# Optimization experiments

Measured on AMD Instinct MI355X. Metric: run time of the kernel, lower is better.

## Reference

```python
import jax, jax.numpy as jnp
import numpy as np

LATENT = 512
HIDDEN = 1024
SLOTS = 16
BATCH = 256
HORIZON = 64


def _linear(x, W, b):
    # torch nn.Linear convention: W [out, in]
    return x @ W.T + b


def _lstm_cell(x, h, c, w_ih, w_hh, b_ih, b_hh):
    # PyTorch gate order: i, f, g, o
    gates = x @ w_ih.T + b_ih + h @ w_hh.T + b_hh
    i, f, g, o = jnp.split(gates, 4, axis=-1)
    i = jax.nn.sigmoid(i)
    f = jax.nn.sigmoid(f)
    g = jnp.tanh(g)
    o = jax.nn.sigmoid(o)
    c_new = f * c + i * g
    h_new = o * jnp.tanh(c_new)
    return h_new, c_new


def setup_inputs() -> dict:
    key = jax.random.key(0)
    ks = iter(jax.random.split(key, 32))

    def rn(shape, scale=None):
        k = next(ks)
        s = scale if scale is not None else 1.0 / np.sqrt(shape[-1])
        return jax.random.normal(k, shape, dtype=jnp.float32) * s

    inp = {
        "current_state": jax.random.normal(next(ks), (BATCH, LATENT), dtype=jnp.float32),
        "horizon": HORIZON,
        # ContextMemory
        "memory": jax.random.normal(next(ks), (SLOTS, HIDDEN), dtype=jnp.float32) * 0.01,
        "q_W": rn((HIDDEN, LATENT)), "q_b": jnp.zeros((HIDDEN,), jnp.float32),
        "k_W": rn((HIDDEN, HIDDEN)), "k_b": jnp.zeros((HIDDEN,), jnp.float32),
        "v_W": rn((HIDDEN, HIDDEN)), "v_b": jnp.zeros((HIDDEN,), jnp.float32),
        "mo_W": rn((LATENT, HIDDEN)), "mo_b": jnp.zeros((LATENT,), jnp.float32),
        # prior_generator: Linear(2L->H), ReLU, Linear(H->L)
        "pg_W1": rn((HIDDEN, 2 * LATENT)), "pg_b1": jnp.zeros((HIDDEN,), jnp.float32),
        "pg_W2": rn((LATENT, HIDDEN)), "pg_b2": jnp.zeros((LATENT,), jnp.float32),
        # LSTM layer 0 (input LATENT) and layer 1 (input HIDDEN)
        "w_ih0": rn((4 * HIDDEN, LATENT)), "w_hh0": rn((4 * HIDDEN, HIDDEN)),
        "b_ih0": jnp.zeros((4 * HIDDEN,), jnp.float32), "b_hh0": jnp.zeros((4 * HIDDEN,), jnp.float32),
        "w_ih1": rn((4 * HIDDEN, HIDDEN)), "w_hh1": rn((4 * HIDDEN, HIDDEN)),
        "b_ih1": jnp.zeros((4 * HIDDEN,), jnp.float32), "b_hh1": jnp.zeros((4 * HIDDEN,), jnp.float32),
        # output_proj: Linear(H->H), ReLU, Linear(H->L)
        "op_W1": rn((HIDDEN, HIDDEN)), "op_b1": jnp.zeros((HIDDEN,), jnp.float32),
        "op_W2": rn((LATENT, HIDDEN)), "op_b2": jnp.zeros((LATENT,), jnp.float32),
    }
    return inp


def reference(current_state, horizon, memory,
              q_W, q_b, k_W, k_b, v_W, v_b, mo_W, mo_b,
              pg_W1, pg_b1, pg_W2, pg_b2,
              w_ih0, w_hh0, b_ih0, b_hh0,
              w_ih1, w_hh1, b_ih1, b_hh1,
              op_W1, op_b1, op_W2, op_b2):
    B = current_state.shape[0]

    # --- ContextMemory.read ---
    q = _linear(current_state, q_W, q_b)          # [B, M]
    k = _linear(memory, k_W, k_b)                 # [S, M]
    v = _linear(memory, v_W, v_b)                 # [S, M]
    scores = (q @ k.T) / jnp.sqrt(jnp.float32(HIDDEN))  # [B, S]
    weights = jax.nn.softmax(scores, axis=-1)
    ctx = weights @ v                             # [B, M]
    context = _linear(ctx, mo_W, mo_b)            # [B, L]

    # --- prior_generator ---
    combined = jnp.concatenate([current_state, context], axis=-1)
    prior = _linear(jax.nn.relu(_linear(combined, pg_W1, pg_b1)), pg_W2, pg_b2)

    h0 = jnp.zeros((B, HIDDEN), jnp.float32)
    c0 = jnp.zeros((B, HIDDEN), jnp.float32)
    h1 = jnp.zeros((B, HIDDEN), jnp.float32)
    c1 = jnp.zeros((B, HIDDEN), jnp.float32)

    def step(carry, _):
        x, h0, c0, h1, c1 = carry
        h0, c0 = _lstm_cell(x, h0, c0, w_ih0, w_hh0, b_ih0, b_hh0)
        h1, c1 = _lstm_cell(h0, h1, c1, w_ih1, w_hh1, b_ih1, b_hh1)
        pred = _linear(jax.nn.relu(_linear(h1, op_W1, op_b1)), op_W2, op_b2)
        return (pred, h0, c0, h1, c1), pred

    _, preds = jax.lax.scan(step, (prior, h0, c0, h1, c1), None, length=horizon)
    predictions = jnp.transpose(preds, (1, 0, 2))  # [B, H, L]
    return predictions, prior
```

## Files before the change

### kernel.cpp

```cpp
#include <hip/hip_runtime.h>
#include <cstddef>
#include <cstdint>

#define LAT 512
#define HID 1024
#define NSLOT 16
#define NB 256
#define HOR 64

using short8  = __attribute__((ext_vector_type(8))) short;
using floatx4 = __attribute__((ext_vector_type(4))) float;

__device__ __forceinline__ float sigmoid_f(float x) { return 1.0f / (1.0f + __expf(-x)); }
__device__ __forceinline__ float tanh_f(float x) {
    float e = __expf(2.0f * x);
    return 1.0f - 2.0f / (e + 1.0f);
}
__device__ __forceinline__ unsigned short f2bf(float f) {
    union { float f; uint32_t u; } v; v.f = f;
    uint32_t u = v.u;
    return (unsigned short)((u + 0x7fffu + ((u >> 16) & 1u)) >> 16);
}
__device__ __forceinline__ void async16(const void* g, void* l) {
    __builtin_amdgcn_global_load_lds(
        (const __attribute__((address_space(1))) unsigned int*)(unsigned long long)g,
        (__attribute__((address_space(3))) unsigned int*)(unsigned int)(unsigned long long)l,
        16, 0, 0);
}

template<int BM, int BN, int MODE>
__global__ __launch_bounds__(512)
void mfma_gemm(const unsigned short* __restrict__ A, int lda,
               const unsigned short* __restrict__ W, int ldw, int K,
               const float* __restrict__ bias,
               float* __restrict__ Cf, int ldc,
               unsigned short* __restrict__ Cb, int ldcb,
               unsigned short* __restrict__ Cb2, int ldcb2)
{
    constexpr int WM = BM / 2, WN = BN / 2, TM = WM / 16, TN = WN / 16;
    static_assert(MODE != 3 || TN == 4, "MODE 3 needs BN=128 (gate quad per thread)");
    __shared__ __attribute__((aligned(16))) short As[2][2][BM * 64];
    __shared__ __attribute__((aligned(16))) short Bs[2][2][BN * 64];

    const int t    = threadIdx.x;
    const int tk   = t >> 8;
    const int lt   = t & 255;
    const int lane = lt & 63;
    const int w    = lt >> 6;
    const int wm   = w >> 1, wn = w & 1;
    const int m0   = blockIdx.y * BM;
    const int n0   = blockIdx.x * BN;
    const int kb   = tk * (K / 2);

    const int r8 = lane >> 3;
    const int cx = (lane & 7) ^ r8;
    const int q  = lane >> 4;
    const int ml = lane & 15;

    floatx4 acc[TM][TN];
    const floatx4 zf = {0.f, 0.f, 0.f, 0.f};
    #pragma unroll
    for (int i = 0; i < TM; ++i)
        #pragma unroll
        for (int j = 0; j < TN; ++j) acc[i][j] = zf;

    auto stage = [&](int k0, int buf) {
        #pragma unroll
        for (int u = 0; u < BM / 32; ++u) {
            const int row = w * (BM / 4) + u * 8;
            async16(A + (size_t)(m0 + row + r8) * lda + k0 + cx * 8, &As[tk][buf][row * 64]);
        }
        #pragma unroll
        for (int u = 0; u < BN / 32; ++u) {
            const int row = w * (BN / 4) + u * 8;
            async16(W + (size_t)(n0 + row + r8) * ldw + k0 + cx * 8, &Bs[tk][buf][row * 64]);
        }
    };

    stage(kb, 0);
    __syncthreads();
    const int nk = (K / 2) / 64;
    for (int it = 0; it < nk; ++it) {
        if (it + 1 < nk) stage(kb + (it + 1) * 64, (it + 1) & 1);
        const short* as = As[tk][it & 1];
        const short* bs = Bs[tk][it & 1];
        #pragma unroll
        for (int s = 0; s < 2; ++s) {
            short8 af[TM], bfr[TN];
            #pragma unroll
            for (int i = 0; i < TM; ++i) {
                const int m = wm * WM + i * 16 + ml;
                af[i] = *(const short8*)&as[(m * 8 + ((s * 4 + q) ^ (m & 7))) * 8];
            }
            #pragma unroll
            for (int j = 0; j < TN; ++j) {
                const int n = wn * WN + j * 16 + ml;
                bfr[j] = *(const short8*)&bs[(n * 8 + ((s * 4 + q) ^ (n & 7))) * 8];
            }
            #pragma unroll
            for (int i = 0; i < TM; ++i)
                #pragma unroll
                for (int j = 0; j < TN; ++j)
                    acc[i][j] = __builtin_amdgcn_mfma_f32_16x16x32_bf16(af[i], bfr[j], acc[i][j], 0, 0, 0);
        }
        __syncthreads();
    }

    floatx4* ex = (floatx4*)&Bs[1][0][0];
    if (tk == 1) {
        #pragma unroll
        for (int i = 0; i < TM; ++i)
            #pragma unroll
            for (int j = 0; j < TN; ++j)
                ex[lt * (TM * TN) + i * TN + j] = acc[i][j];
    }
    __syncthreads();
    if (tk == 1) return;
    #pragma unroll
    for (int i = 0; i < TM; ++i)
        #pragma unroll
        for (int j = 0; j < TN; ++j) {
            const floatx4 o = ex[lt * (TM * TN) + i * TN + j];
            acc[i][j][0] += o[0]; acc[i][j][1] += o[1];
            acc[i][j][2] += o[2]; acc[i][j][3] += o[3];
        }

    const int gmb = m0 + wm * WM + q * 4;
    if constexpr (MODE == 3) {
        const int nn = n0 + wn * WN;
        const int jj = (nn >> 6) * 16 + ml;
        const float bI = bias[nn + ml],      bF = bias[nn + 16 + ml];
        const float bG = bias[nn + 32 + ml], bO = bias[nn + 48 + ml];
        #pragma unroll
        for (int i = 0; i < TM; ++i)
            #pragma unroll
            for (int r = 0; r < 4; ++r) {
                const int b = gmb + i * 16 + r;
                const float i_ = sigmoid_f(acc[i][0][r] + bI);
                const float f_ = sigmoid_f(acc[i][1][r] + bF);
                const float g_ = tanh_f(acc[i][2][r] + bG);
                const float o_ = sigmoid_f(acc[i][3][r] + bO);
                float* cp = Cf + (size_t)b * ldc + jj;
                const float cn = f_ * (*cp) + i_ * g_;
                *cp = cn;
                const unsigned short hb = f2bf(o_ * tanh_f(cn));
                Cb[(size_t)b * ldcb + jj] = hb;
                if (Cb2) Cb2[(size_t)b * ldcb2 + jj] = hb;
            }
    } else {
        const int gnb = n0 + wn * WN + ml;
        #pragma unroll
        for (int i = 0; i < TM; ++i)
            #pragma unroll
            for (int j = 0; j < TN; ++j) {
                const int gm = gmb + i * 16, gn = gnb + j * 16;
                const float bv = bias[gn];
                #pragma unroll
                for (int r = 0; r < 4; ++r) {
                    float v = acc[i][j][r] + bv;
                    if (MODE == 1) v = fmaxf(v, 0.f);
                    if (MODE == 2) Cf[(size_t)(gm + r) * ldc + gn] = v;
                    Cb[(size_t)(gm + r) * ldcb + gn] = f2bf(v);
                }
            }
    }
}

__global__ __launch_bounds__(256)
void pack_gates(const float* __restrict__ w_ih, int Kih,
                const float* __restrict__ w_hh, int Khh,
                const float* __restrict__ b_ih, const float* __restrict__ b_hh,
                unsigned short* __restrict__ d, float* __restrict__ bc, int K)
{
    const int idx = blockIdx.x * 256 + threadIdx.x;
    if (idx >= 4096 * K) return;
    const int p = idx / K;
    const int k = idx - p * K;
    const int g = (p >> 4) & 3;
    const int j = ((p >> 6) << 4) | (p & 15);
    const int orow = g * 1024 + j;
    const float v = (k < Kih) ? w_ih[(size_t)orow * Kih + k]
                              : w_hh[(size_t)orow * Khh + (k - Kih)];
    d[idx] = f2bf(v);
    if (k == 0) bc[p] = b_ih[orow] + b_hh[orow];
}

__global__ __launch_bounds__(256)
void pack2(const float* __restrict__ s1, int K1, const float* __restrict__ s2, int K2,
           unsigned short* __restrict__ d, int total, int K)
{
    const int idx = blockIdx.x * 256 + threadIdx.x;
    if (idx >= total) return;
    const int n = idx / K;
    const int k = idx - n * K;
    const float v = (k < K1) ? s1[(size_t)n * K1 + k] : s2[(size_t)n * K2 + (k - K1)];
    d[idx] = f2bf(v);
}

template<int RELU>
__global__ __launch_bounds__(256)
void gemm_tn(const float* __restrict__ A1, int lda1,
             const float* __restrict__ W1, int ldw1, int K1,
             const float* __restrict__ A2, int lda2,
             const float* __restrict__ W2, int ldw2, int K2,
             const float* __restrict__ bias1,
             float* __restrict__ C, int ldc,
             unsigned short* __restrict__ C2, int ldc2,
             int M, int N)
{
    __shared__ float As[16][64];
    __shared__ float Ws[16][64];
    const int t   = threadIdx.x;
    const int bn0 = blockIdx.x * 64;
    const int bm0 = blockIdx.y * 64;
    const int tx  = t & 15;
    const int ty  = t >> 4;
    const int lr  = t >> 2;
    const int lc  = (t & 3) << 2;

    float acc[4][4] = {};

    for (int src = 0; src < 2; ++src) {
        const float* A = src ? A2 : A1;
        if (!A) continue;
        const float* W = src ? W2 : W1;
        const int lda = src ? lda2 : lda1;
        const int ldw = src ? ldw2 : ldw1;
        const int K   = src ? K2 : K1;
        for (int k0 = 0; k0 < K; k0 += 16) {
            float4 av = make_float4(0.f, 0.f, 0.f, 0.f);
            const int am = bm0 + lr;
            if (am < M) av = *(const float4*)(A + (size_t)am * lda + k0 + lc);
            const float4 wv = *(const float4*)(W + (size_t)(bn0 + lr) * ldw + k0 + lc);
            __syncthreads();
            As[lc + 0][lr] = av.x; As[lc + 1][lr] = av.y;
            As[lc + 2][lr] = av.z; As[lc + 3][lr] = av.w;
            Ws[lc + 0][lr] = wv.x; Ws[lc + 1][lr] = wv.y;
            Ws[lc + 2][lr] = wv.z; Ws[lc + 3][lr] = wv.w;
            __syncthreads();
            #pragma unroll
            for (int kk = 0; kk < 16; ++kk) {
                const float4 a = *(const float4*)&As[kk][ty * 4];
                const float4 b = *(const float4*)&Ws[kk][tx * 4];
                const float ar[4] = {a.x, a.y, a.z, a.w};
                const float br[4] = {b.x, b.y, b.z, b.w};
                #pragma unroll
                for (int i = 0; i < 4; ++i)
                    #pragma unroll
                    for (int j = 0; j < 4; ++j)
                        acc[i][j] = fmaf(ar[i], br[j], acc[i][j]);
            }
        }
    }

    const int n0 = bn0 + tx * 4;
    float bv[4] = {0.f, 0.f, 0.f, 0.f};
    if (bias1) {
        #pragma unroll
        for (int j = 0; j < 4; ++j) bv[j] += bias1[n0 + j];
    }
    #pragma unroll
    for (int i = 0; i < 4; ++i) {
        const int m = bm0 + ty * 4 + i;
        if (m < M) {
            float ov[4];
            #pragma unroll
            for (int j = 0; j < 4; ++j) {
                float v = acc[i][j] + bv[j];
                if (RELU) v = fmaxf(v, 0.f);
                ov[j] = v;
            }
            *(float4*)(C + (size_t)m * ldc + n0) = make_float4(ov[0], ov[1], ov[2], ov[3]);
            if (C2) {
                #pragma unroll
                for (int j = 0; j < 4; ++j)
                    C2[(size_t)m * ldc2 + n0 + j] = f2bf(ov[j]);
            }
        }
    }
}

__global__ __launch_bounds__(256)
void attn_kernel(const float* __restrict__ q, const float* __restrict__ k,
                 const float* __restrict__ v, float* __restrict__ ctx)
{
    __shared__ float red[NSLOT][4];
    __shared__ float wts[NSLOT];
    const int b = blockIdx.x;
    const int t = threadIdx.x;
    const float4 qv = *(const float4*)(q + (size_t)b * HID + t * 4);
    #pragma unroll
    for (int s = 0; s < NSLOT; ++s) {
        const float4 kv = *(const float4*)(k + (size_t)s * HID + t * 4);
        float p = qv.x * kv.x + qv.y * kv.y + qv.z * kv.z + qv.w * kv.w;
        #pragma unroll
        for (int off = 32; off > 0; off >>= 1) p += __shfl_down(p, off);
        if ((t & 63) == 0) red[s][t >> 6] = p;
    }
    __syncthreads();
    if (t == 0) {
        float sc[NSLOT];
        float mx = -1e30f;
        for (int s = 0; s < NSLOT; ++s) {
            sc[s] = (red[s][0] + red[s][1] + red[s][2] + red[s][3]) * 0.03125f;
            mx = fmaxf(mx, sc[s]);
        }
        float sum = 0.f;
        for (int s = 0; s < NSLOT; ++s) { const float e = __expf(sc[s] - mx); wts[s] = e; sum += e; }
        const float inv = 1.f / sum;
        for (int s = 0; s < NSLOT; ++s) wts[s] *= inv;
    }
    __syncthreads();
    float4 a = make_float4(0.f, 0.f, 0.f, 0.f);
    #pragma unroll
    for (int s = 0; s < NSLOT; ++s) {
        const float wv = wts[s];
        const float4 vv = *(const float4*)(v + (size_t)s * HID + t * 4);
        a.x += wv * vv.x; a.y += wv * vv.y; a.z += wv * vv.z; a.w += wv * vv.w;
    }
    *(float4*)(ctx + (size_t)b * HID + t * 4) = a;
}

extern "C" void kernel_launch(void* const* d_in, const int* in_sizes, int n_in,
                              void* d_out, int out_size, void* d_ws, size_t ws_size,
                              hipStream_t stream)
{
    const float* cs    = (const float*)d_in[0];
    const float* mem   = (const float*)d_in[2];
    const float* q_W   = (const float*)d_in[3];
    const float* q_b   = (const float*)d_in[4];
    const float* k_W   = (const float*)d_in[5];
    const float* k_b   = (const float*)d_in[6];
    const float* v_W   = (const float*)d_in[7];
    const float* v_b   = (const float*)d_in[8];
    const float* mo_W  = (const float*)d_in[9];
    const float* mo_b  = (const float*)d_in[10];
    const float* pg_W1 = (const float*)d_in[11];
    const float* pg_b1 = (const float*)d_in[12];
    const float* pg_W2 = (const float*)d_in[13];
    const float* pg_b2 = (const float*)d_in[14];
    const float* w_ih0 = (const float*)d_in[15];
    const float* w_hh0 = (const float*)d_in[16];
    const float* b_ih0 = (const float*)d_in[17];
    const float* b_hh0 = (const float*)d_in[18];
    const float* w_ih1 = (const float*)d_in[19];
    const float* w_hh1 = (const float*)d_in[20];
    const float* b_ih1 = (const float*)d_in[21];
    const float* b_hh1 = (const float*)d_in[22];
    const float* op_W1 = (const float*)d_in[23];
    const float* op_b1 = (const float*)d_in[24];
    const float* op_W2 = (const float*)d_in[25];
    const float* op_b2 = (const float*)d_in[26];

    float* out       = (float*)d_out;
    float* prior_out = out + (size_t)NB * HOR * LAT;

    char* base = (char*)d_ws;
    auto alloc = [&](size_t bytes) { char* r = base; base += (bytes + 255) & ~255ull; return r; };

    unsigned short* Wg0p = (unsigned short*)alloc((size_t)4 * HID * (LAT + HID) * 2);
    unsigned short* Wg1p = (unsigned short*)alloc((size_t)4 * HID * (2 * HID) * 2);
    unsigned short* Wo1  = (unsigned short*)alloc((size_t)HID * HID * 2);
    unsigned short* Wo2  = (unsigned short*)alloc((size_t)LAT * HID * 2);
    float*          bc0  = (float*)alloc((size_t)4 * HID * 4);
    float*          bc1  = (float*)alloc((size_t)4 * HID * 4);
    unsigned short* xh0  = (unsigned short*)alloc((size_t)2 * NB * (LAT + HID) * 2);
    unsigned short* hh1  = (unsigned short*)alloc((size_t)2 * NB * (2 * HID) * 2);
    float*          c0   = (float*)alloc((size_t)NB * HID * 4);
    float*          c1   = (float*)alloc((size_t)NB * HID * 4);
    unsigned short* tbuf = (unsigned short*)alloc((size_t)NB * HID * 2);
    float* qbuf   = (float*)alloc((size_t)NB * HID * 4);
    float* kbuf   = (float*)alloc((size_t)NSLOT * HID * 4);
    float* vbuf   = (float*)alloc((size_t)NSLOT * HID * 4);
    float* ctxbuf = (float*)alloc((size_t)NB * HID * 4);
    float* ctxo   = (float*)alloc((size_t)NB * LAT * 4);
    float* pgh    = (float*)alloc((size_t)NB * HID * 4);

    const size_t zbytes = (size_t)2 * NB * (LAT + HID) * 2
                        + (size_t)2 * NB * (2 * HID) * 2
                        + (size_t)NB * HID * 4 * 2;
    hipMemsetAsync(xh0, 0, zbytes, stream);

    const dim3 blk(256);
    const dim3 blk512(512);

    {
        int tot = 4 * HID * (LAT + HID);
        pack_gates<<<dim3((tot + 255) / 256), blk, 0, stream>>>(
            w_ih0, LAT, w_hh0, HID, b_ih0, b_hh0, Wg0p, bc0, LAT + HID);
        tot = 4 * HID * (2 * HID);
        pack_gates<<<dim3((tot + 255) / 256), blk, 0, stream>>>(
            w_ih1, HID, w_hh1, HID, b_ih1, b_hh1, Wg1p, bc1, 2 * HID);
        tot = HID * HID;
        pack2<<<dim3((tot + 255) / 256), blk, 0, stream>>>(op_W1, HID, nullptr, 0, Wo1, tot, HID);
        tot = LAT * HID;
        pack2<<<dim3((tot + 255) / 256), blk, 0, stream>>>(op_W2, HID, nullptr, 0, Wo2, tot, HID);
    }

    gemm_tn<0><<<dim3(HID / 64, 1), blk, 0, stream>>>(
        mem, HID, k_W, HID, HID, nullptr, 0, nullptr, 0, 0,
        k_b, kbuf, HID, nullptr, 0, NSLOT, HID);
    gemm_tn<0><<<dim3(HID / 64, 1), blk, 0, stream>>>(
        mem, HID, v_W, HID, HID, nullptr, 0, nullptr, 0, 0,
        v_b, vbuf, HID, nullptr, 0, NSLOT, HID);
    gemm_tn<0><<<dim3(HID / 64, NB / 64), blk, 0, stream>>>(
        cs, LAT, q_W, LAT, LAT, nullptr, 0, nullptr, 0, 0,
        q_b, qbuf, HID, nullptr, 0, NB, HID);
    attn_kernel<<<dim3(NB), blk, 0, stream>>>(qbuf, kbuf, vbuf, ctxbuf);
    gemm_tn<0><<<dim3(LAT / 64, NB / 64), blk, 0, stream>>>(
        ctxbuf, HID, mo_W, HID, HID, nullptr, 0, nullptr, 0, 0,
        mo_b, ctxo, LAT, nullptr, 0, NB, LAT);
    gemm_tn<1><<<dim3(HID / 64, NB / 64), blk, 0, stream>>>(
        cs, LAT, pg_W1, HID, LAT, ctxo, LAT, pg_W1 + LAT, HID, LAT,
        pg_b1, pgh, HID, nullptr, 0, NB, HID);
    gemm_tn<0><<<dim3(LAT / 64, NB / 64), blk, 0, stream>>>(
        pgh, HID, pg_W2, HID, HID, nullptr, 0, nullptr, 0, 0,
        pg_b2, prior_out, LAT, xh0, LAT + HID, NB, LAT);

    for (int step = 0; step < HOR; ++step) {
        const int cur = step & 1, nxt = cur ^ 1;
        unsigned short* xh_r = xh0 + (size_t)cur * NB * (LAT + HID);
        unsigned short* xh_w = xh0 + (size_t)nxt * NB * (LAT + HID);
        unsigned short* hh_c = hh1 + (size_t)cur * NB * (2 * HID);
        unsigned short* hh_n = hh1 + (size_t)nxt * NB * (2 * HID);

        mfma_gemm<64, 128, 3><<<dim3(4 * HID / 128, NB / 64), blk512, 0, stream>>>(
            xh_r, LAT + HID, Wg0p, LAT + HID, LAT + HID,
            bc0, c0, HID, hh_c, 2 * HID, xh_w + LAT, LAT + HID);
        mfma_gemm<64, 128, 3><<<dim3(4 * HID / 128, NB / 64), blk512, 0, stream>>>(
            hh_c, 2 * HID, Wg1p, 2 * HID, 2 * HID,
            bc1, c1, HID, hh_n + HID, 2 * HID, nullptr, 0);
        mfma_gemm<64, 64, 1><<<dim3(HID / 64, NB / 64), blk512, 0, stream>>>(
            hh_n + HID, 2 * HID, Wo1, HID, HID,
            op_b1, nullptr, 0, tbuf, HID, nullptr, 0);
        mfma_gemm<64, 64, 2><<<dim3(LAT / 64, NB / 64), blk512, 0, stream>>>(
            tbuf, HID, Wo2, HID, HID,
            op_b2, out + (size_t)step * LAT, HOR * LAT, xh_w, LAT + HID, nullptr, 0);
    }
}
```

Baseline: 3.783 ms.

## Fuse LSTM rollout into one persistent cooperative kernel with grid barriers

Replaces the 256 per-step GEMM launches of the autoregressive rollout with a single cooperative kernel of 128 blocks. Each block runs the four GEMM phases in turn and separates them with a custom hierarchical atomic grid barrier. This is meant to remove kernel launch and drain overhead between the small dependent GEMMs. The cost is that blocks sit idle during the smaller output-projection phases, and correctness now depends on all blocks being co-resident and on the barrier's memory ordering.

```diff
diff --git a/kernel.cpp b/kernel.cpp
--- a/kernel.cpp
+++ b/kernel.cpp
@@ -29,27 +29,22 @@
 }
 
 template<int BM, int BN, int MODE>
-__global__ __launch_bounds__(512)
-void mfma_gemm(const unsigned short* __restrict__ A, int lda,
-               const unsigned short* __restrict__ W, int ldw, int K,
-               const float* __restrict__ bias,
-               float* __restrict__ Cf, int ldc,
-               unsigned short* __restrict__ Cb, int ldcb,
-               unsigned short* __restrict__ Cb2, int ldcb2)
+__device__ __forceinline__ void gemm_phase(
+    const unsigned short* __restrict__ A, int lda,
+    const unsigned short* __restrict__ W, int ldw, int K,
+    const float* __restrict__ bias,
+    float* __restrict__ Cf, int ldc,
+    unsigned short* __restrict__ Cb, int ldcb,
+    unsigned short* __restrict__ Cb2, int ldcb2,
+    int m0, int n0, short* AsL, short* BsL, int t)
 {
     constexpr int WM = BM / 2, WN = BN / 2, TM = WM / 16, TN = WN / 16;
-    static_assert(MODE != 3 || TN == 4, "MODE 3 needs BN=128 (gate quad per thread)");
-    __shared__ __attribute__((aligned(16))) short As[2][2][BM * 64];
-    __shared__ __attribute__((aligned(16))) short Bs[2][2][BN * 64];
-
-    const int t    = threadIdx.x;
+    static_assert(MODE != 3 || TN == 4, "MODE 3 needs BN=128");
     const int tk   = t >> 8;
     const int lt   = t & 255;
     const int lane = lt & 63;
     const int w    = lt >> 6;
     const int wm   = w >> 1, wn = w & 1;
-    const int m0   = blockIdx.y * BM;
-    const int n0   = blockIdx.x * BN;
     const int kb   = tk * (K / 2);
 
     const int r8 = lane >> 3;
@@ -57,6 +52,9 @@
     const int q  = lane >> 4;
     const int ml = lane & 15;
 
+    short* Ast = AsL + tk * (2 * BM * 64);
+    short* Bst = BsL + tk * (2 * BN * 64);
+
     floatx4 acc[TM][TN];
     const floatx4 zf = {0.f, 0.f, 0.f, 0.f};
     #pragma unroll
@@ -65,15 +63,17 @@
         for (int j = 0; j < TN; ++j) acc[i][j] = zf;
 
     auto stage = [&](int k0, int buf) {
+        short* ad = Ast + buf * (BM * 64);
+        short* bd = Bst + buf * (BN * 64);
         #pragma unroll
         for (int u = 0; u < BM / 32; ++u) {
             const int row = w * (BM / 4) + u * 8;
-            async16(A + (size_t)(m0 + row + r8) * lda + k0 + cx * 8, &As[tk][buf][row * 64]);
+            async16(A + (size_t)(m0 + row + r8) * lda + k0 + cx * 8, ad + row * 64);
         }
         #pragma unroll
         for (int u = 0; u < BN / 32; ++u) {
             const int row = w * (BN / 4) + u * 8;
-            async16(W + (size_t)(n0 + row + r8) * ldw + k0 + cx * 8, &Bs[tk][buf][row * 64]);
+            async16(W + (size_t)(n0 + row + r8) * ldw + k0 + cx * 8, bd + row * 64);
         }
     };
 
@@ -82,8 +82,8 @@
     const int nk = (K / 2) / 64;
     for (int it = 0; it < nk; ++it) {
         if (it + 1 < nk) stage(kb + (it + 1) * 64, (it + 1) & 1);
-        const short* as = As[tk][it & 1];
-        const short* bs = Bs[tk][it & 1];
+        const short* as = Ast + (it & 1) * (BM * 64);
+        const short* bs = Bst + (it & 1) * (BN * 64);
         #pragma unroll
         for (int s = 0; s < 2; ++s) {
             short8 af[TM], bfr[TN];
@@ -106,7 +106,7 @@
         __syncthreads();
     }
 
-    floatx4* ex = (floatx4*)&Bs[1][0][0];
+    floatx4* ex = (floatx4*)(BsL + 2 * BN * 64);
     if (tk == 1) {
         #pragma unroll
         for (int i = 0; i < TM; ++i)
@@ -115,54 +115,137 @@
                 ex[lt * (TM * TN) + i * TN + j] = acc[i][j];
     }
     __syncthreads();
-    if (tk == 1) return;
-    #pragma unroll
-    for (int i = 0; i < TM; ++i)
-        #pragma unroll
-        for (int j = 0; j < TN; ++j) {
-            const floatx4 o = ex[lt * (TM * TN) + i * TN + j];
-            acc[i][j][0] += o[0]; acc[i][j][1] += o[1];
-            acc[i][j][2] += o[2]; acc[i][j][3] += o[3];
-        }
-
-    const int gmb = m0 + wm * WM + q * 4;
-    if constexpr (MODE == 3) {
-        const int nn = n0 + wn * WN;
-        const int jj = (nn >> 6) * 16 + ml;
-        const float bI = bias[nn + ml],      bF = bias[nn + 16 + ml];
-        const float bG = bias[nn + 32 + ml], bO = bias[nn + 48 + ml];
+    if (tk == 0) {
         #pragma unroll
         for (int i = 0; i < TM; ++i)
             #pragma unroll
-            for (int r = 0; r < 4; ++r) {
-                const int b = gmb + i * 16 + r;
-                const float i_ = sigmoid_f(acc[i][0][r] + bI);
-                const float f_ = sigmoid_f(acc[i][1][r] + bF);
-                const float g_ = tanh_f(acc[i][2][r] + bG);
-                const float o_ = sigmoid_f(acc[i][3][r] + bO);
-                float* cp = Cf + (size_t)b * ldc + jj;
-                const float cn = f_ * (*cp) + i_ * g_;
-                *cp = cn;
-                const unsigned short hb = f2bf(o_ * tanh_f(cn));
-                Cb[(size_t)b * ldcb + jj] = hb;
-                if (Cb2) Cb2[(size_t)b * ldcb2 + jj] = hb;
+            for (int j = 0; j < TN; ++j) {
+                const floatx4 o = ex[lt * (TM * TN) + i * TN + j];
+                acc[i][j][0] += o[0]; acc[i][j][1] += o[1];
+                acc[i][j][2] += o[2]; acc[i][j][3] += o[3];
             }
-    } else {
-        const int gnb = n0 + wn * WN + ml;
-        #pragma unroll
-        for (int i = 0; i < TM; ++i)
-            #pragma unroll
-            for (int j = 0; j < TN; ++j) {
-                const int gm = gmb + i * 16, gn = gnb + j * 16;
-                const float bv = bias[gn];
+
+        const int gmb = m0 + wm * WM + q * 4;
+        if constexpr (MODE == 3) {
+            const int nn = n0 + wn * WN;
+            const int jj = (nn >> 6) * 16 + ml;
+            const float bI = bias[nn + ml],      bF = bias[nn + 16 + ml];
+            const float bG = bias[nn + 32 + ml], bO = bias[nn + 48 + ml];
+            #pragma unroll
+            for (int i = 0; i < TM; ++i)
                 #pragma unroll
                 for (int r = 0; r < 4; ++r) {
-                    float v = acc[i][j][r] + bv;
-                    if (MODE == 1) v = fmaxf(v, 0.f);
-                    if (MODE == 2) Cf[(size_t)(gm + r) * ldc + gn] = v;
-                    Cb[(size_t)(gm + r) * ldcb + gn] = f2bf(v);
+                    const int b = gmb + i * 16 + r;
+                    const float i_ = sigmoid_f(acc[i][0][r] + bI);
+                    const float f_ = sigmoid_f(acc[i][1][r] + bF);
+                    const float g_ = tanh_f(acc[i][2][r] + bG);
+                    const float o_ = sigmoid_f(acc[i][3][r] + bO);
+                    float* cp = Cf + (size_t)b * ldc + jj;
+                    const float cn = f_ * (*cp) + i_ * g_;
+                    *cp = cn;
+                    const unsigned short hb = f2bf(o_ * tanh_f(cn));
+                    Cb[(size_t)b * ldcb + jj] = hb;
+                    if (Cb2) Cb2[(size_t)b * ldcb2 + jj] = hb;
                 }
-            }
+        } else {
+            const int gnb = n0 + wn * WN + ml;
+            #pragma unroll
+            for (int i = 0; i < TM; ++i)
+                #pragma unroll
+                for (int j = 0; j < TN; ++j) {
+                    const int gm = gmb + i * 16, gn = gnb + j * 16;
+                    const float bv = bias[gn];
+                    #pragma unroll
+                    for (int r = 0; r < 4; ++r) {
+                        float v = acc[i][j][r] + bv;
+                        if (MODE == 1) v = fmaxf(v, 0.f);
+                        if (MODE == 2) Cf[(size_t)(gm + r) * ldc + gn] = v;
+                        Cb[(size_t)(gm + r) * ldcb + gn] = f2bf(v);
+                    }
+                }
+        }
+    }
+    __syncthreads();
+}
+
+__device__ __forceinline__ void gridbar(unsigned* bar, int round)
+{
+    __syncthreads();
+    if (threadIdx.x == 0) {
+        __threadfence();
+        unsigned old = atomicAdd(&bar[(blockIdx.x & 7) << 6], 1u);
+        if (old == (unsigned)round * 16u - 1u)
+            atomicAdd(&bar[512], 1u);
+        while (__hip_atomic_load(&bar[512], __ATOMIC_RELAXED, __HIP_MEMORY_SCOPE_AGENT)
+               < (unsigned)round * 8u)
+            __builtin_amdgcn_s_sleep(2);
+        __threadfence();
+    }
+    __syncthreads();
+}
+
+struct RollArgs {
+    const unsigned short* Wg0;
+    const unsigned short* Wg1;
+    const unsigned short* Wo1;
+    const unsigned short* Wo2;
+    const float* bc0;
+    const float* bc1;
+    const float* ob1;
+    const float* ob2;
+    unsigned short* xh0;
+    unsigned short* hh1;
+    float* c0;
+    float* c1;
+    unsigned short* tbuf;
+    float* out;
+    unsigned* bar;
+};
+
+__global__ __launch_bounds__(512)
+void rollout(RollArgs a)
+{
+    __shared__ __attribute__((aligned(16))) short AsL[2 * 2 * 64 * 64];
+    __shared__ __attribute__((aligned(16))) short BsL[2 * 2 * 128 * 64];
+
+    const int t   = threadIdx.x;
+    const int blk = blockIdx.x;
+    const int nb  = blk >> 2;
+    const int mb  = blk & 3;
+    int round = 0;
+
+    for (int step = 0; step < HOR; ++step) {
+        const int cur = step & 1, nxt = cur ^ 1;
+        unsigned short* xh_r = a.xh0 + (size_t)cur * NB * (LAT + HID);
+        unsigned short* xh_w = a.xh0 + (size_t)nxt * NB * (LAT + HID);
+        unsigned short* hh_c = a.hh1 + (size_t)cur * NB * (2 * HID);
+        unsigned short* hh_n = a.hh1 + (size_t)nxt * NB * (2 * HID);
+
+        gemm_phase<64, 128, 3>(
+            xh_r, LAT + HID, a.Wg0, LAT + HID, LAT + HID,
+            a.bc0, a.c0, HID, hh_c, 2 * HID, xh_w + LAT, LAT + HID,
+            mb * 64, nb * 128, AsL, BsL, t);
+        gridbar(a.bar, ++round);
+
+        gemm_phase<64, 128, 3>(
+            hh_c, 2 * HID, a.Wg1, 2 * HID, 2 * HID,
+            a.bc1, a.c1, HID, hh_n + HID, 2 * HID, nullptr, 0,
+            mb * 64, nb * 128, AsL, BsL, t);
+        gridbar(a.bar, ++round);
+
+        if (blk < 64)
+            gemm_phase<64, 64, 1>(
+                hh_n + HID, 2 * HID, a.Wo1, HID, HID,
+                a.ob1, nullptr, 0, a.tbuf, HID, nullptr, 0,
+                mb * 64, nb * 64, AsL, BsL, t);
+        gridbar(a.bar, ++round);
+
+        if (blk < 32)
+            gemm_phase<64, 64, 2>(
+                a.tbuf, HID, a.Wo2, HID, HID,
+                a.ob2, a.out + (size_t)step * LAT, HOR * LAT, xh_w, LAT + HID, nullptr, 0,
+                mb * 64, nb * 64, AsL, BsL, t);
+        gridbar(a.bar, ++round);
     }
 }
 
@@ -368,6 +451,7 @@
     unsigned short* hh1  = (unsigned short*)alloc((size_t)2 * NB * (2 * HID) * 2);
     float*          c0   = (float*)alloc((size_t)NB * HID * 4);
     float*          c1   = (float*)alloc((size_t)NB * HID * 4);
+    unsigned*       bar  = (unsigned*)alloc(4096);
     unsigned short* tbuf = (unsigned short*)alloc((size_t)NB * HID * 2);
     float* qbuf   = (float*)alloc((size_t)NB * HID * 4);
     float* kbuf   = (float*)alloc((size_t)NSLOT * HID * 4);
@@ -378,11 +462,10 @@
 
     const size_t zbytes = (size_t)2 * NB * (LAT + HID) * 2
                         + (size_t)2 * NB * (2 * HID) * 2
-                        + (size_t)NB * HID * 4 * 2;
+                        + (size_t)NB * HID * 4 * 2 + 4096;
     hipMemsetAsync(xh0, 0, zbytes, stream);
 
     const dim3 blk(256);
-    const dim3 blk512(512);
 
     {
         int tot = 4 * HID * (LAT + HID);
@@ -417,24 +500,11 @@
         pgh, HID, pg_W2, HID, HID, nullptr, 0, nullptr, 0, 0,
         pg_b2, prior_out, LAT, xh0, LAT + HID, NB, LAT);
 
-    for (int step = 0; step < HOR; ++step) {
-        const int cur = step & 1, nxt = cur ^ 1;
-        unsigned short* xh_r = xh0 + (size_t)cur * NB * (LAT + HID);
-        unsigned short* xh_w = xh0 + (size_t)nxt * NB * (LAT + HID);
-        unsigned short* hh_c = hh1 + (size_t)cur * NB * (2 * HID);
-        unsigned short* hh_n = hh1 + (size_t)nxt * NB * (2 * HID);
-
-        mfma_gemm<64, 128, 3><<<dim3(4 * HID / 128, NB / 64), blk512, 0, stream>>>(
-            xh_r, LAT + HID, Wg0p, LAT + HID, LAT + HID,
-            bc0, c0, HID, hh_c, 2 * HID, xh_w + LAT, LAT + HID);
-        mfma_gemm<64, 128, 3><<<dim3(4 * HID / 128, NB / 64), blk512, 0, stream>>>(
-            hh_c, 2 * HID, Wg1p, 2 * HID, 2 * HID,
-            bc1, c1, HID, hh_n + HID, 2 * HID, nullptr, 0);
-        mfma_gemm<64, 64, 1><<<dim3(HID / 64, NB / 64), blk512, 0, stream>>>(
-            hh_n + HID, 2 * HID, Wo1, HID, HID,
-            op_b1, nullptr, 0, tbuf, HID, nullptr, 0);
-        mfma_gemm<64, 64, 2><<<dim3(LAT / 64, NB / 64), blk512, 0, stream>>>(
-            tbuf, HID, Wo2, HID, HID,
-            op_b2, out + (size_t)step * LAT, HOR * LAT, xh_w, LAT + HID, nullptr, 0);
-    }
-}
+    RollArgs ra;
+    ra.Wg0 = Wg0p; ra.Wg1 = Wg1p; ra.Wo1 = Wo1; ra.Wo2 = Wo2;
+    ra.bc0 = bc0;  ra.bc1 = bc1;  ra.ob1 = op_b1; ra.ob2 = op_b2;
+    ra.xh0 = xh0;  ra.hh1 = hh1;  ra.c0 = c0; ra.c1 = c1;
+    ra.tbuf = tbuf; ra.out = out; ra.bar = bar;
+    void* kargs[] = { (void*)&ra };
+    hipLaunchCooperativeKernel((const void*)rollout, dim3(128), dim3(512), kargs, 0, stream);
+}
```

New measurement: 6.928 ms. 1.83x slower.

## Generalize split-K teams to four per block and shrink LSTM gate tile M

Applied to the files above, without the earlier changes.

Makes the number of in-block split-K teams a template parameter and raises it from two to four, using 1024-thread blocks, with a per-team LDS staging area and a multi-source reduction at the end. The LSTM gate GEMMs also move from BM=64 to BM=32, which doubles their block count. The aim is more parallelism for these small, latency-bound per-step GEMMs at batch 256, so more CUs and waves stay busy. In exchange it adds LDS use per block and a longer reduction tail, and shorter K loops per team give less room to pipeline.

```diff
diff --git a/kernel.cpp b/kernel.cpp
--- a/kernel.cpp
+++ b/kernel.cpp
@@ -28,8 +28,8 @@
         16, 0, 0);
 }
 
-template<int BM, int BN, int MODE>
-__global__ __launch_bounds__(512)
+template<int BM, int BN, int MODE, int TEAMS>
+__global__ __launch_bounds__(TEAMS * 256)
 void mfma_gemm(const unsigned short* __restrict__ A, int lda,
                const unsigned short* __restrict__ W, int ldw, int K,
                const float* __restrict__ bias,
@@ -39,8 +39,8 @@
 {
     constexpr int WM = BM / 2, WN = BN / 2, TM = WM / 16, TN = WN / 16;
     static_assert(MODE != 3 || TN == 4, "MODE 3 needs BN=128 (gate quad per thread)");
-    __shared__ __attribute__((aligned(16))) short As[2][2][BM * 64];
-    __shared__ __attribute__((aligned(16))) short Bs[2][2][BN * 64];
+    __shared__ __attribute__((aligned(16))) short As[TEAMS * 2 * BM * 64];
+    __shared__ __attribute__((aligned(16))) short Bs[TEAMS * 2 * BN * 64];
 
     const int t    = threadIdx.x;
     const int tk   = t >> 8;
@@ -50,13 +50,16 @@
     const int wm   = w >> 1, wn = w & 1;
     const int m0   = blockIdx.y * BM;
     const int n0   = blockIdx.x * BN;
-    const int kb   = tk * (K / 2);
+    const int kb   = tk * (K / TEAMS);
 
     const int r8 = lane >> 3;
     const int cx = (lane & 7) ^ r8;
     const int q  = lane >> 4;
     const int ml = lane & 15;
 
+    short* Ast = As + tk * (2 * BM * 64);
+    short* Bst = Bs + tk * (2 * BN * 64);
+
     floatx4 acc[TM][TN];
     const floatx4 zf = {0.f, 0.f, 0.f, 0.f};
     #pragma unroll
@@ -65,25 +68,27 @@
         for (int j = 0; j < TN; ++j) acc[i][j] = zf;
 
     auto stage = [&](int k0, int buf) {
+        short* ad = Ast + buf * (BM * 64);
+        short* bd = Bst + buf * (BN * 64);
         #pragma unroll
         for (int u = 0; u < BM / 32; ++u) {
             const int row = w * (BM / 4) + u * 8;
-            async16(A + (size_t)(m0 + row + r8) * lda + k0 + cx * 8, &As[tk][buf][row * 64]);
+            async16(A + (size_t)(m0 + row + r8) * lda + k0 + cx * 8, ad + row * 64);
         }
         #pragma unroll
         for (int u = 0; u < BN / 32; ++u) {
             const int row = w * (BN / 4) + u * 8;
-            async16(W + (size_t)(n0 + row + r8) * ldw + k0 + cx * 8, &Bs[tk][buf][row * 64]);
+            async16(W + (size_t)(n0 + row + r8) * ldw + k0 + cx * 8, bd + row * 64);
         }
     };
 
     stage(kb, 0);
     __syncthreads();
-    const int nk = (K / 2) / 64;
+    const int nk = (K / TEAMS) / 64;
     for (int it = 0; it < nk; ++it) {
         if (it + 1 < nk) stage(kb + (it + 1) * 64, (it + 1) & 1);
-        const short* as = As[tk][it & 1];
-        const short* bs = Bs[tk][it & 1];
+        const short* as = Ast + (it & 1) * (BM * 64);
+        const short* bs = Bst + (it & 1) * (BN * 64);
         #pragma unroll
         for (int s = 0; s < 2; ++s) {
             short8 af[TM], bfr[TN];
@@ -106,8 +111,8 @@
         __syncthreads();
     }
 
-    floatx4* ex = (floatx4*)&Bs[1][0][0];
-    if (tk == 1) {
+    if (tk > 0) {
+        floatx4* ex = (floatx4*)(Bs + (size_t)tk * (2 * BN * 64));
         #pragma unroll
         for (int i = 0; i < TM; ++i)
             #pragma unroll
@@ -115,15 +120,19 @@
                 ex[lt * (TM * TN) + i * TN + j] = acc[i][j];
     }
     __syncthreads();
-    if (tk == 1) return;
+    if (tk != 0) return;
     #pragma unroll
-    for (int i = 0; i < TM; ++i)
-        #pragma unroll
-        for (int j = 0; j < TN; ++j) {
-            const floatx4 o = ex[lt * (TM * TN) + i * TN + j];
-            acc[i][j][0] += o[0]; acc[i][j][1] += o[1];
-            acc[i][j][2] += o[2]; acc[i][j][3] += o[3];
-        }
+    for (int src = 1; src < TEAMS; ++src) {
+        const floatx4* ex = (const floatx4*)(Bs + (size_t)src * (2 * BN * 64));
+        #pragma unroll
+        for (int i = 0; i < TM; ++i)
+            #pragma unroll
+            for (int j = 0; j < TN; ++j) {
+                const floatx4 o = ex[lt * (TM * TN) + i * TN + j];
+                acc[i][j][0] += o[0]; acc[i][j][1] += o[1];
+                acc[i][j][2] += o[2]; acc[i][j][3] += o[3];
+            }
+    }
 
     const int gmb = m0 + wm * WM + q * 4;
     if constexpr (MODE == 3) {
@@ -382,7 +391,7 @@
     hipMemsetAsync(xh0, 0, zbytes, stream);
 
     const dim3 blk(256);
-    const dim3 blk512(512);
+    const dim3 blk1k(1024);
 
     {
         int tot = 4 * HID * (LAT + HID);
@@ -424,16 +433,16 @@
         unsigned short* hh_c = hh1 + (size_t)cur * NB * (2 * HID);
         unsigned short* hh_n = hh1 + (size_t)nxt * NB * (2 * HID);
 
-        mfma_gemm<64, 128, 3><<<dim3(4 * HID / 128, NB / 64), blk512, 0, stream>>>(
+        mfma_gemm<32, 128, 3, 4><<<dim3(4 * HID / 128, NB / 32), blk1k, 0, stream>>>(
             xh_r, LAT + HID, Wg0p, LAT + HID, LAT + HID,
             bc0, c0, HID, hh_c, 2 * HID, xh_w + LAT, LAT + HID);
-        mfma_gemm<64, 128, 3><<<dim3(4 * HID / 128, NB / 64), blk512, 0, stream>>>(
+        mfma_gemm<32, 128, 3, 4><<<dim3(4 * HID / 128, NB / 32), blk1k, 0, stream>>>(
             hh_c, 2 * HID, Wg1p, 2 * HID, 2 * HID,
             bc1, c1, HID, hh_n + HID, 2 * HID, nullptr, 0);
-        mfma_gemm<64, 64, 1><<<dim3(HID / 64, NB / 64), blk512, 0, stream>>>(
+        mfma_gemm<64, 64, 1, 4><<<dim3(HID / 64, NB / 64), blk1k, 0, stream>>>(
             hh_n + HID, 2 * HID, Wo1, HID, HID,
             op_b1, nullptr, 0, tbuf, HID, nullptr, 0);
-        mfma_gemm<64, 64, 2><<<dim3(LAT / 64, NB / 64), blk512, 0, stream>>>(
+        mfma_gemm<64, 64, 2, 4><<<dim3(LAT / 64, NB / 64), blk1k, 0, stream>>>(
             tbuf, HID, Wo2, HID, HID,
             op_b2, out + (size_t)step * LAT, HOR * LAT, xh_w, LAT + HID, nullptr, 0);
     }
```

Result: faster. 3.078 ms (-18.6%).
